# Kernel tuning notes

Hardware: AMD Instinct MI355X
Metric: run time of the kernel (lower is better)

The kernel has to match this reference:

```python
import jax, jax.numpy as jnp
import numpy as np

V, D, H, S = 100000, 300, 300, 4096   # vocab, embed dim, biLSTM hidden (2x150), seq len
HU = H // 2                            # per-direction LSTM units
NSYN = 4


def _lstm(x, W, U, b):
    """Keras-style LSTM scan. x: [S, D] -> hidden states [S, HU]. Gate order i,f,g,o."""
    def step(carry, xt):
        h, c = carry
        z = xt @ W + h @ U + b              # [4*HU]
        i, f, g, o = jnp.split(z, 4)
        i = jax.nn.sigmoid(i)
        f = jax.nn.sigmoid(f)
        g = jnp.tanh(g)
        o = jax.nn.sigmoid(o)
        c = f * c + i * g
        h = o * jnp.tanh(c)
        return (h, c), h
    init = (jnp.zeros((HU,), x.dtype), jnp.zeros((HU,), x.dtype))
    _, hs = jax.lax.scan(step, init, x)
    return hs


def setup_inputs() -> dict:
    key = jax.random.key(0)
    ks = jax.random.split(key, 20)
    s = 0.05  # small init scale keeps exp() attention scores well-conditioned
    return {
        "sentence": jax.random.randint(ks[0], (S,), 0, V),
        "synonym_indices": jax.random.randint(ks[1], (S, NSYN), 0, V),
        "embedding_matrix": jax.random.normal(ks[2], (V, D), jnp.float32) * s,
        # forward-direction LSTM
        "W_f": jax.random.normal(ks[3], (D, 4 * HU), jnp.float32) * s,
        "U_f": jax.random.normal(ks[4], (HU, 4 * HU), jnp.float32) * s,
        "b_f": jnp.zeros((4 * HU,), jnp.float32),
        # backward-direction LSTM
        "W_b": jax.random.normal(ks[5], (D, 4 * HU), jnp.float32) * s,
        "U_b": jax.random.normal(ks[6], (HU, 4 * HU), jnp.float32) * s,
        "b_b": jnp.zeros((4 * HU,), jnp.float32),
        # primary attention dense (h1 -> h1)
        "W_p": jax.random.normal(ks[7], (H, H), jnp.float32) * s,
        "b_p": jnp.zeros((H,), jnp.float32),
        # secondary attention dense (2*h1 -> 1, tanh)
        "W_s": jax.random.normal(ks[8], (2 * H, 1), jnp.float32) * s,
        "b_s": jnp.zeros((1,), jnp.float32),
        # output heads
        "W_emo": jax.random.normal(ks[9], (2 * H, 8), jnp.float32) * s,
        "b_emo": jnp.zeros((8,), jnp.float32),
        "W_sent": jax.random.normal(ks[10], (2 * H, 1), jnp.float32) * s,
        "b_sent": jnp.zeros((1,), jnp.float32),
    }


def reference(sentence, synonym_indices, embedding_matrix,
              W_f, U_f, b_f, W_b, U_b, b_b,
              W_p, b_p, W_s, b_s, W_emo, b_emo, W_sent, b_sent):
    emb = embedding_matrix[sentence]                       # [S, D] gather
    # bidirectional LSTM (concat fwd and reversed-bwd hidden states)
    h_fwd = _lstm(emb, W_f, U_f, b_f)                      # [S, HU]
    h_bwd = _lstm(emb[::-1], W_b, U_b, b_b)[::-1]          # [S, HU]
    hidden_states = jnp.concatenate([h_fwd, h_bwd], -1)    # [S, H]
    # primary attention: per-word synonym gather + exp-scored weighted sum (vectorized)
    out = hidden_states @ W_p + b_p                        # [S, H]
    syn = embedding_matrix[synonym_indices]                # [S, NSYN, D] irregular gather
    scores = jnp.exp(jnp.einsum('sd,skd->sk', out, syn))   # [S, NSYN]
    m = jnp.einsum('sk,skd->sd', scores, syn)              # [S, D]
    h_hats = jnp.concatenate([hidden_states, m], -1)       # [S, 2H]
    # secondary attention
    coeff = jnp.exp(jnp.tanh(h_hats @ W_s + b_s))          # [S, 1]
    H_HAT = jnp.sum(coeff * h_hats, axis=0)[None, :]       # [1, 2H]
    emotion_logits = H_HAT @ W_emo + b_emo                 # [1, 8]
    sentiment_logits = H_HAT @ W_sent + b_sent             # [1, 1]
    return (emotion_logits, sentiment_logits)
```

## Files before the change

kernel.cpp:

```cpp
#include <hip/hip_runtime.h>
#include <hip/hip_bf16.h>
#include <math.h>

#define S_LEN 4096
#define D_EMB 300
#define NG    600
#define HDIM  300
#define H2    600
#define VOCAB 100000

typedef float v4f __attribute__((ext_vector_type(4)));
typedef _Float16 f16x2 __attribute__((ext_vector_type(2)));
typedef _Float16 f16x8 __attribute__((ext_vector_type(8)));

__device__ __forceinline__ float bf2f(unsigned short u) {
  union { unsigned int i; float f; } v; v.i = ((unsigned int)u) << 16; return v.f;
}
__device__ __forceinline__ unsigned short f2bf(float f) {
  union { float f; unsigned int i; } v; v.f = f;
  return (unsigned short)((v.i + 0x7FFFu + ((v.i >> 16) & 1u)) >> 16);
}

__device__ __forceinline__ void bar_lds() {
  asm volatile("s_waitcnt lgkmcnt(0)\n\ts_barrier" ::: "memory");
}

__global__ void zero_hh(float* __restrict__ HH) {
  if (threadIdx.x < 640) HH[threadIdx.x] = 0.f;
}
__global__ void zero_out_f(float* __restrict__ o, int n) {
  if ((int)threadIdx.x < n) o[threadIdx.x] = 0.f;
}

#define BM 64
#define BN 64
#define BK 16
template<bool A_BF16>
__global__ __launch_bounds__(256) void gemm_bias(
    const void* __restrict__ Av,
    const int* __restrict__ idx, int lda, int nrowsA,
    const float* __restrict__ B,
    const float* __restrict__ bias,
    unsigned short* __restrict__ C,
    int N, int K)
{
  __shared__ __align__(16) float As[BK][BM + 4];
  __shared__ __align__(16) float Bs[BK][BN + 4];
  __shared__ int rowidx[BM];

  int tid = threadIdx.x;
  int bm0 = blockIdx.y * BM, bn0 = blockIdx.x * BN;
  if (tid < BM) {
    int r = idx ? idx[bm0 + tid] : (bm0 + tid);
    r = (r < 0) ? 0 : ((r >= nrowsA) ? (nrowsA - 1) : r);
    rowidx[tid] = r;
  }
  __syncthreads();

  int tx  = tid & 15, ty = tid >> 4;
  int ar  = tid >> 2, akv = (tid & 3) << 2;
  int bkr = tid >> 4, bnv = (tid & 15) << 2;

  float acc[4][4] = {};
  for (int kk = 0; kk < K; kk += BK) {
    float a0=0.f, a1=0.f, a2=0.f, a3=0.f;
    int ka = kk + akv;
    if (ka < K) {
      if (A_BF16) {
        const unsigned short* A = (const unsigned short*)Av;
        ushort4 qa = *(const ushort4*)(A + (size_t)rowidx[ar]*lda + ka);
        a0 = bf2f(qa.x); a1 = bf2f(qa.y); a2 = bf2f(qa.z); a3 = bf2f(qa.w);
      } else {
        const float* A = (const float*)Av;
        float4 qa = *(const float4*)(A + (size_t)rowidx[ar]*lda + ka);
        a0 = qa.x; a1 = qa.y; a2 = qa.z; a3 = qa.w;
      }
    }
    float b0=0.f, b1=0.f, b2=0.f, b3=0.f;
    int kb = kk + bkr, nb = bn0 + bnv;
    if (kb < K && nb < N) {
      float4 qb = *(const float4*)(B + (size_t)kb*N + nb);
      b0 = qb.x; b1 = qb.y; b2 = qb.z; b3 = qb.w;
    }
    As[akv+0][ar] = a0; As[akv+1][ar] = a1; As[akv+2][ar] = a2; As[akv+3][ar] = a3;
    Bs[bkr][bnv+0] = b0; Bs[bkr][bnv+1] = b1; Bs[bkr][bnv+2] = b2; Bs[bkr][bnv+3] = b3;
    __syncthreads();
    #pragma unroll
    for (int k = 0; k < BK; ++k) {
      v4f av = *(const v4f*)&As[k][ty << 2];
      v4f bv = *(const v4f*)&Bs[k][tx << 2];
      #pragma unroll
      for (int i = 0; i < 4; ++i)
        #pragma unroll
        for (int j = 0; j < 4; ++j)
          acc[i][j] += av[i] * bv[j];
    }
    __syncthreads();
  }
  #pragma unroll
  for (int i = 0; i < 4; ++i) {
    int m = bm0 + (ty << 2) + i;
    #pragma unroll
    for (int j = 0; j < 4; ++j) {
      int n = bn0 + (tx << 2) + j;
      if (n < N) C[(size_t)m*N + n] = f2bf(acc[i][j] + bias[n]);
    }
  }
}

__global__ __launch_bounds__(640) void lstm_kernel(
    const unsigned short* __restrict__ pre_f, const unsigned short* __restrict__ pre_b,
    const float* __restrict__ Uf, const float* __restrict__ Ub,
    unsigned short* __restrict__ hidden )
{
  const int dir = blockIdx.x;
  const unsigned short* pre = dir ? pre_b : pre_f;
  const float* U            = dir ? Ub : Uf;
  const int tid  = threadIdx.x;
  const int wave = tid >> 6, lane = tid & 63;

  __shared__ __align__(16) unsigned short h_u16[160];
  __shared__ __align__(16) float zrow[608];
  __shared__ __align__(16) unsigned short h_hist[8][160];

  const bool bc = tid < 150;

  const int ncnt   = (wave < 2) ? 3 : 4;
  const int nstart = (wave < 2) ? 3 * wave : 6 + 4 * (wave - 2);

  const int bgrp = lane >> 4;
  const int bn   = lane & 15;

  f16x8 bfr[4][5];
  #pragma unroll
  for (int t = 0; t < 4; ++t) {
    #pragma unroll
    for (int kt = 0; kt < 5; ++kt) {
      f16x8 v;
      #pragma unroll
      for (int e = 0; e < 8; ++e) {
        int row = (kt << 5) + (bgrp << 3) + e;
        int col = ((nstart + t) << 4) + bn;
        float x = (t < ncnt && row < 150 && col < 600) ? U[(size_t)row*600 + col] : 0.f;
        v[e] = (_Float16)x;
      }
      bfr[t][kt] = v;
    }
  }

  const int t0 = dir ? (S_LEN - 1) : 0;
  const int dt = dir ? -1 : 1;
  const ptrdiff_t pstep = (ptrdiff_t)dt * 600;

  if (tid < 160) h_u16[tid] = 0;

  float pA0=0,pA1=0,pA2=0,pA3=0, pB0=0,pB1=0,pB2=0,pB3=0;
  const unsigned short* pre2 = pre + (ptrdiff_t)t0*600 + 2*pstep;
  if (bc) {
    const unsigned short* g0 = pre + (ptrdiff_t)t0*600;
    pA0 = bf2f(g0[tid]); pA1 = bf2f(g0[tid+150]);
    pA2 = bf2f(g0[tid+300]); pA3 = bf2f(g0[tid+450]);
    const unsigned short* g1 = g0 + pstep;
    pB0 = bf2f(g1[tid]); pB1 = bf2f(g1[tid+150]);
    pB2 = bf2f(g1[tid+300]); pB3 = bf2f(g1[tid+450]);
  }
  float c = 0.f;
  __syncthreads();

  const _Float16* hf = (const _Float16*)h_u16;

  for (int s8 = 0; s8 < S_LEN/8; ++s8) {
    if (s8 && tid < 600) {
      int sub = tid / 75, w = (tid % 75) << 1;
      int sp  = (s8 << 3) - 8 + sub;
      int tp  = dir ? (S_LEN - 1 - sp) : sp;
      *(unsigned int*)(hidden + (size_t)tp*300 + dir*150 + w) =
          *(const unsigned int*)&h_hist[sub][w];
    }
    #pragma unroll
    for (int ss = 0; ss < 8; ++ss) {
      const int s = (s8 << 3) + ss;
      float pC0=0,pC1=0,pC2=0,pC3=0;
      if (bc && s + 2 < S_LEN) {
        pC0 = bf2f(pre2[tid]);       pC1 = bf2f(pre2[tid+150]);
        pC2 = bf2f(pre2[tid+300]);   pC3 = bf2f(pre2[tid+450]);
      }
      {
        v4f a0 = {0.f,0.f,0.f,0.f}, a1 = a0, a2 = a0, a3 = a0;
        #pragma unroll
        for (int kt = 0; kt < 5; ++kt) {
          f16x8 av = *(const f16x8*)&hf[(kt << 5) + (bgrp << 3)];
          a0 = __builtin_amdgcn_mfma_f32_16x16x32_f16(av, bfr[0][kt], a0, 0, 0, 0);
          a1 = __builtin_amdgcn_mfma_f32_16x16x32_f16(av, bfr[1][kt], a1, 0, 0, 0);
          a2 = __builtin_amdgcn_mfma_f32_16x16x32_f16(av, bfr[2][kt], a2, 0, 0, 0);
          if (ncnt == 4)
            a3 = __builtin_amdgcn_mfma_f32_16x16x32_f16(av, bfr[3][kt], a3, 0, 0, 0);
        }
        if (lane < 16) {
          int base = (nstart << 4) + bn;
          zrow[base]      = a0[0];
          zrow[base + 16] = a1[0];
          zrow[base + 32] = a2[0];
          if (ncnt == 4) zrow[base + 48] = a3[0];
        }
      }
      bar_lds();

      if (bc) {
        float zi = pA0 + zrow[tid];
        float zff= pA1 + zrow[150 + tid];
        float zg = pA2 + zrow[300 + tid];
        float zo = pA3 + zrow[450 + tid];
        float gi = __builtin_amdgcn_rcpf(1.f + __expf(-zi));
        float gf = __builtin_amdgcn_rcpf(1.f + __expf(-zff));
        float gg = 1.f - 2.f * __builtin_amdgcn_rcpf(__expf(2.f * zg) + 1.f);
        float go = __builtin_amdgcn_rcpf(1.f + __expf(-zo));
        c = gf * c + gi * gg;
        float th = 1.f - 2.f * __builtin_amdgcn_rcpf(__expf(2.f * c) + 1.f);
        float hv = go * th;
        ((_Float16*)h_u16)[tid] = (_Float16)hv;
        h_hist[ss][tid] = f2bf(hv);
        pA0 = pB0; pA1 = pB1; pA2 = pB2; pA3 = pB3;
        pB0 = pC0; pB1 = pC1; pB2 = pC2; pB3 = pC3;
      }
      bar_lds();
      pre2 += pstep;
    }
  }

  if (tid < 600) {
    int sub = tid / 75, w = (tid % 75) << 1;
    int sp  = S_LEN - 8 + sub;
    int tp  = dir ? (S_LEN - 1 - sp) : sp;
    *(unsigned int*)(hidden + (size_t)tp*300 + dir*150 + w) =
        *(const unsigned int*)&h_hist[sub][w];
  }
}

__global__ __launch_bounds__(128) void attn_word(
    const unsigned short* __restrict__ outp,
    const unsigned short* __restrict__ hid,
    const float* __restrict__ E,
    const int* __restrict__ syn,
    const float* __restrict__ W_s,
    const float* __restrict__ b_s,
    float* __restrict__ HH)
{
  int t = blockIdx.x, tid = threadIdx.x;
  __shared__ float s_out[300], s_hid[300], s_syn[4][300], s_m[300];
  __shared__ float s_red[8], s_sc[4], s_cf;

  int r0 = syn[t*4+0], r1 = syn[t*4+1], r2 = syn[t*4+2], r3 = syn[t*4+3];
  r0 = (r0 < 0) ? 0 : ((r0 >= VOCAB) ? VOCAB-1 : r0);
  r1 = (r1 < 0) ? 0 : ((r1 >= VOCAB) ? VOCAB-1 : r1);
  r2 = (r2 < 0) ? 0 : ((r2 >= VOCAB) ? VOCAB-1 : r2);
  r3 = (r3 < 0) ? 0 : ((r3 >= VOCAB) ? VOCAB-1 : r3);
  for (int d = tid; d < 300; d += 128) {
    s_out[d] = bf2f(outp[(size_t)t*300 + d]);
    s_hid[d] = bf2f(hid[(size_t)t*300 + d]);
    s_syn[0][d] = E[(size_t)r0*300 + d];
    s_syn[1][d] = E[(size_t)r1*300 + d];
    s_syn[2][d] = E[(size_t)r2*300 + d];
    s_syn[3][d] = E[(size_t)r3*300 + d];
  }
  __syncthreads();

  float p0=0.f, p1=0.f, p2=0.f, p3=0.f;
  for (int d = tid; d < 300; d += 128) {
    float o = s_out[d];
    p0 += o*s_syn[0][d]; p1 += o*s_syn[1][d];
    p2 += o*s_syn[2][d]; p3 += o*s_syn[3][d];
  }
  #pragma unroll
  for (int off = 32; off; off >>= 1) {
    p0 += __shfl_down(p0, off); p1 += __shfl_down(p1, off);
    p2 += __shfl_down(p2, off); p3 += __shfl_down(p3, off);
  }
  int wave = tid >> 6, lane = tid & 63;
  if (lane == 0) {
    s_red[wave*4+0] = p0; s_red[wave*4+1] = p1;
    s_red[wave*4+2] = p2; s_red[wave*4+3] = p3;
  }
  __syncthreads();
  if (tid < 4) s_sc[tid] = __expf(fminf(s_red[tid] + s_red[4 + tid], 50.f));
  __syncthreads();

  float sc0 = s_sc[0], sc1 = s_sc[1], sc2 = s_sc[2], sc3 = s_sc[3];
  float cp = 0.f;
  for (int d = tid; d < 300; d += 128) {
    float m = sc0*s_syn[0][d] + sc1*s_syn[1][d] + sc2*s_syn[2][d] + sc3*s_syn[3][d];
    s_m[d] = m;
    cp += s_hid[d]*W_s[d] + m*W_s[300 + d];
  }
  #pragma unroll
  for (int off = 32; off; off >>= 1) cp += __shfl_down(cp, off);
  if (lane == 0) s_red[wave] = cp;
  __syncthreads();
  if (tid == 0) s_cf = __expf(tanhf(s_red[0] + s_red[1] + b_s[0]));
  __syncthreads();

  float cf = s_cf;
  for (int d = tid; d < 300; d += 128) {
    atomicAdd(&HH[d],       cf * s_hid[d]);
    atomicAdd(&HH[300 + d], cf * s_m[d]);
  }
}

__global__ void heads(const float* __restrict__ HH,
                      const float* __restrict__ W_emo, const float* __restrict__ b_emo,
                      const float* __restrict__ W_sent, const float* __restrict__ b_sent,
                      float* __restrict__ out) {
  int tid = threadIdx.x;
  if (tid < 8) {
    float a = 0.f;
    for (int d = 0; d < H2; ++d) a += HH[d] * W_emo[d*8 + tid];
    out[tid] = a + b_emo[tid];
  } else if (tid == 8) {
    float a = 0.f;
    for (int d = 0; d < H2; ++d) a += HH[d] * W_sent[d];
    out[8] = a + b_sent[0];
  }
}

extern "C" void kernel_launch(void* const* d_in, const int* in_sizes, int n_in,
                              void* d_out, int out_size, void* d_ws, size_t ws_size,
                              hipStream_t stream) {
  const int*   sentence = (const int*)d_in[0];
  const int*   syn_idx  = (const int*)d_in[1];
  const float* E        = (const float*)d_in[2];
  const float* W_f      = (const float*)d_in[3];
  const float* U_f      = (const float*)d_in[4];
  const float* b_f      = (const float*)d_in[5];
  const float* W_b      = (const float*)d_in[6];
  const float* U_b      = (const float*)d_in[7];
  const float* b_b      = (const float*)d_in[8];
  const float* W_p      = (const float*)d_in[9];
  const float* b_p      = (const float*)d_in[10];
  const float* W_s      = (const float*)d_in[11];
  const float* b_s      = (const float*)d_in[12];
  const float* W_emo    = (const float*)d_in[13];
  const float* b_emo    = (const float*)d_in[14];
  const float* W_sent   = (const float*)d_in[15];
  const float* b_sent   = (const float*)d_in[16];
  float*       outv     = (float*)d_out;

  unsigned char* ws = (unsigned char*)d_ws;
  float*          HH     = (float*)ws;
  unsigned short* hidden = (unsigned short*)(ws + 2560);
  unsigned short* out_p  = (unsigned short*)(ws + 2460160);
  unsigned short* pre_f  = (unsigned short*)(ws + 4917760);
  unsigned short* pre_b  = (unsigned short*)(ws + 9832960);

  if (ws_size < 14748160u) {
    zero_out_f<<<1, 64, 0, stream>>>(outv, out_size);
    return;
  }

  zero_hh<<<1, 640, 0, stream>>>(HH);
  gemm_bias<false><<<dim3(10, 64), 256, 0, stream>>>(
      (const void*)E, sentence, D_EMB, VOCAB, W_f, b_f, pre_f, NG, D_EMB);
  gemm_bias<false><<<dim3(10, 64), 256, 0, stream>>>(
      (const void*)E, sentence, D_EMB, VOCAB, W_b, b_b, pre_b, NG, D_EMB);
  lstm_kernel<<<2, 640, 0, stream>>>(pre_f, pre_b, U_f, U_b, hidden);
  gemm_bias<true><<<dim3(5, 64), 256, 0, stream>>>(
      (const void*)hidden, nullptr, HDIM, S_LEN, W_p, b_p, out_p, HDIM, HDIM);
  attn_word<<<S_LEN, 128, 0, stream>>>(out_p, hidden, E, syn_idx, W_s, b_s, HH);
  heads<<<1, 64, 0, stream>>>(HH, W_emo, b_emo, W_sent, b_sent, outv);
}
```

Baseline: 3.740 ms.

## Remap LSTM gate columns per wave to drop zrow exchange and one barrier

```diff
diff --git a/kernel.cpp b/kernel.cpp
--- a/kernel.cpp
+++ b/kernel.cpp
@@ -119,32 +119,28 @@
   const int tid  = threadIdx.x;
   const int wave = tid >> 6, lane = tid & 63;
 
-  __shared__ __align__(16) unsigned short h_u16[160];
-  __shared__ __align__(16) float zrow[608];
-  __shared__ __align__(16) unsigned short h_hist[8][160];
-
-  const bool bc = tid < 150;
-
-  const int ncnt   = (wave < 2) ? 3 : 4;
-  const int nstart = (wave < 2) ? 3 * wave : 6 + 4 * (wave - 2);
-
+  __shared__ __align__(16) unsigned short h2[2][160];
+  __shared__ __align__(16) unsigned short h_hist[2][8][160];
+
+  const int bn   = lane & 15;
   const int bgrp = lane >> 4;
-  const int bn   = lane & 15;
+  const int cell = wave * 16 + bn;
+  const bool own = (lane < 16) && (cell < 150);
 
   f16x8 bfr[4][5];
   #pragma unroll
-  for (int t = 0; t < 4; ++t) {
+  for (int g = 0; g < 4; ++g) {
     #pragma unroll
     for (int kt = 0; kt < 5; ++kt) {
       f16x8 v;
       #pragma unroll
       for (int e = 0; e < 8; ++e) {
         int row = (kt << 5) + (bgrp << 3) + e;
-        int col = ((nstart + t) << 4) + bn;
-        float x = (t < ncnt && row < 150 && col < 600) ? U[(size_t)row*600 + col] : 0.f;
+        int col = g * 150 + cell;
+        float x = (cell < 150 && row < 150) ? U[(size_t)row*600 + col] : 0.f;
         v[e] = (_Float16)x;
       }
-      bfr[t][kt] = v;
+      bfr[g][kt] = v;
     }
   }
 
@@ -152,78 +148,68 @@
   const int dt = dir ? -1 : 1;
   const ptrdiff_t pstep = (ptrdiff_t)dt * 600;
 
-  if (tid < 160) h_u16[tid] = 0;
+  if (tid < 320) ((unsigned short*)h2)[tid] = 0;
 
   float pA0=0,pA1=0,pA2=0,pA3=0, pB0=0,pB1=0,pB2=0,pB3=0;
   const unsigned short* pre2 = pre + (ptrdiff_t)t0*600 + 2*pstep;
-  if (bc) {
+  if (own) {
     const unsigned short* g0 = pre + (ptrdiff_t)t0*600;
-    pA0 = bf2f(g0[tid]); pA1 = bf2f(g0[tid+150]);
-    pA2 = bf2f(g0[tid+300]); pA3 = bf2f(g0[tid+450]);
+    pA0 = bf2f(g0[cell]); pA1 = bf2f(g0[cell+150]);
+    pA2 = bf2f(g0[cell+300]); pA3 = bf2f(g0[cell+450]);
     const unsigned short* g1 = g0 + pstep;
-    pB0 = bf2f(g1[tid]); pB1 = bf2f(g1[tid+150]);
-    pB2 = bf2f(g1[tid+300]); pB3 = bf2f(g1[tid+450]);
+    pB0 = bf2f(g1[cell]); pB1 = bf2f(g1[cell+150]);
+    pB2 = bf2f(g1[cell+300]); pB3 = bf2f(g1[cell+450]);
   }
   float c = 0.f;
   __syncthreads();
 
-  const _Float16* hf = (const _Float16*)h_u16;
-
+  int p = 0;
   for (int s8 = 0; s8 < S_LEN/8; ++s8) {
+    const int hb = s8 & 1;
     if (s8 && tid < 600) {
       int sub = tid / 75, w = (tid % 75) << 1;
       int sp  = (s8 << 3) - 8 + sub;
       int tp  = dir ? (S_LEN - 1 - sp) : sp;
       *(unsigned int*)(hidden + (size_t)tp*300 + dir*150 + w) =
-          *(const unsigned int*)&h_hist[sub][w];
+          *(const unsigned int*)&h_hist[hb ^ 1][sub][w];
     }
     #pragma unroll
     for (int ss = 0; ss < 8; ++ss) {
       const int s = (s8 << 3) + ss;
       float pC0=0,pC1=0,pC2=0,pC3=0;
-      if (bc && s + 2 < S_LEN) {
-        pC0 = bf2f(pre2[tid]);       pC1 = bf2f(pre2[tid+150]);
-        pC2 = bf2f(pre2[tid+300]);   pC3 = bf2f(pre2[tid+450]);
-      }
-      {
-        v4f a0 = {0.f,0.f,0.f,0.f}, a1 = a0, a2 = a0, a3 = a0;
-        #pragma unroll
-        for (int kt = 0; kt < 5; ++kt) {
-          f16x8 av = *(const f16x8*)&hf[(kt << 5) + (bgrp << 3)];
-          a0 = __builtin_amdgcn_mfma_f32_16x16x32_f16(av, bfr[0][kt], a0, 0, 0, 0);
-          a1 = __builtin_amdgcn_mfma_f32_16x16x32_f16(av, bfr[1][kt], a1, 0, 0, 0);
-          a2 = __builtin_amdgcn_mfma_f32_16x16x32_f16(av, bfr[2][kt], a2, 0, 0, 0);
-          if (ncnt == 4)
-            a3 = __builtin_amdgcn_mfma_f32_16x16x32_f16(av, bfr[3][kt], a3, 0, 0, 0);
-        }
-        if (lane < 16) {
-          int base = (nstart << 4) + bn;
-          zrow[base]      = a0[0];
-          zrow[base + 16] = a1[0];
-          zrow[base + 32] = a2[0];
-          if (ncnt == 4) zrow[base + 48] = a3[0];
-        }
-      }
-      bar_lds();
-
-      if (bc) {
-        float zi = pA0 + zrow[tid];
-        float zff= pA1 + zrow[150 + tid];
-        float zg = pA2 + zrow[300 + tid];
-        float zo = pA3 + zrow[450 + tid];
+      if (own && s + 2 < S_LEN) {
+        pC0 = bf2f(pre2[cell]);       pC1 = bf2f(pre2[cell+150]);
+        pC2 = bf2f(pre2[cell+300]);   pC3 = bf2f(pre2[cell+450]);
+      }
+      const _Float16* hf = (const _Float16*)h2[p];
+      v4f a0 = {0.f,0.f,0.f,0.f}, a1 = a0, a2 = a0, a3 = a0;
+      #pragma unroll
+      for (int kt = 0; kt < 5; ++kt) {
+        f16x8 av = *(const f16x8*)&hf[(kt << 5) + (bgrp << 3)];
+        a0 = __builtin_amdgcn_mfma_f32_16x16x32_f16(av, bfr[0][kt], a0, 0, 0, 0);
+        a1 = __builtin_amdgcn_mfma_f32_16x16x32_f16(av, bfr[1][kt], a1, 0, 0, 0);
+        a2 = __builtin_amdgcn_mfma_f32_16x16x32_f16(av, bfr[2][kt], a2, 0, 0, 0);
+        a3 = __builtin_amdgcn_mfma_f32_16x16x32_f16(av, bfr[3][kt], a3, 0, 0, 0);
+      }
+      if (own) {
+        float zi = pA0 + a0[0];
+        float zf = pA1 + a1[0];
+        float zg = pA2 + a2[0];
+        float zo = pA3 + a3[0];
         float gi = __builtin_amdgcn_rcpf(1.f + __expf(-zi));
-        float gf = __builtin_amdgcn_rcpf(1.f + __expf(-zff));
+        float gf = __builtin_amdgcn_rcpf(1.f + __expf(-zf));
         float gg = 1.f - 2.f * __builtin_amdgcn_rcpf(__expf(2.f * zg) + 1.f);
         float go = __builtin_amdgcn_rcpf(1.f + __expf(-zo));
         c = gf * c + gi * gg;
         float th = 1.f - 2.f * __builtin_amdgcn_rcpf(__expf(2.f * c) + 1.f);
         float hv = go * th;
-        ((_Float16*)h_u16)[tid] = (_Float16)hv;
-        h_hist[ss][tid] = f2bf(hv);
+        ((_Float16*)h2[p ^ 1])[cell] = (_Float16)hv;
+        h_hist[hb][ss][cell] = f2bf(hv);
         pA0 = pB0; pA1 = pB1; pA2 = pB2; pA3 = pB3;
         pB0 = pC0; pB1 = pC1; pB2 = pC2; pB3 = pC3;
       }
       bar_lds();
+      p ^= 1;
       pre2 += pstep;
     }
   }
@@ -233,7 +219,7 @@
     int sp  = S_LEN - 8 + sub;
     int tp  = dir ? (S_LEN - 1 - sp) : sp;
     *(unsigned int*)(hidden + (size_t)tp*300 + dir*150 + w) =
-        *(const unsigned int*)&h_hist[sub][w];
+        *(const unsigned int*)&h_hist[1][sub][w];
   }
 }
 
```

Result: slower. 4.427 ms (+18.4%).
